# Optimization experiments

Measured on AMD Instinct MI355X. Metric: run time of the kernel, lower is better.

Reference implementation:

```python
import jax, jax.numpy as jnp
import numpy as np


def setup_inputs() -> dict:
    key = jax.random.key(0)
    k = jax.random.split(key, 6)
    N, F, C = 8192, 64, 10
    scale = 1.0 / np.sqrt(F)  # keep activations bounded through relu chain
    return {
        "A_tilde": jax.random.uniform(k[0], (N, N), dtype=jnp.float32),
        "emb": jax.random.normal(k[1], (N, F), dtype=jnp.float32),
        "W1": jax.random.normal(k[2], (F, F), dtype=jnp.float32) * scale,
        "W2": jax.random.normal(k[3], (F, F), dtype=jnp.float32) * scale,
        "Wc": jax.random.normal(k[4], (F, C), dtype=jnp.float32) * scale,
        "bc": jnp.zeros((C,), dtype=jnp.float32),
    }


def reference(A_tilde, emb, W1, W2, Wc, bc):
    # D_tilde = rowsum(A)^(-1/2), with inf -> 0 (nan_to_num posinf=0)
    s = A_tilde.sum(axis=1)
    d = jnp.where(s > 0, jax.lax.rsqrt(jnp.where(s > 0, s, 1.0)), 0.0)  # [N]
    x = emb
    for W in (W1, W2):
        hw = x @ W                          # [N, F] = H W
        # DAD @ HW computed as d * (A @ (d * HW)) -- same math as
        # diag(d) @ A @ diag(d) @ HW, without materializing NxN products
        x = jax.nn.relu(d[:, None] * (A_tilde @ (d[:, None] * hw)))
        # dropout is identity in eval mode
    logits = x @ Wc + bc                    # [N, C]
    return logits
```

## Files before the change

### kernel.cpp

```cpp
#include <hip/hip_runtime.h>
#include <stdint.h>

#define N 8192
#define FD 64
#define NC 10
#define SK 8
#define BM 128
#define BK 128

typedef __attribute__((ext_vector_type(8))) __bf16 bf16x8;
typedef __attribute__((ext_vector_type(4))) float f32x4;
typedef __attribute__((ext_vector_type(4))) float vf4;

__device__ __forceinline__ unsigned short f2bf(float f) {
    unsigned u = __builtin_bit_cast(unsigned, f);
    u += 0x7fffu + ((u >> 16) & 1u);
    return (unsigned short)(u >> 16);
}

__device__ __forceinline__ void g2l16(const void* g, void* l) {
    __builtin_amdgcn_global_load_lds(
        (const __attribute__((address_space(1))) unsigned int*)g,
        (__attribute__((address_space(3))) unsigned int*)l, 16, 0, 0);
}

__global__ __launch_bounds__(256) void rowsum_cast(const float* __restrict__ A,
                                                   unsigned short* __restrict__ Abf,
                                                   float* __restrict__ dvec) {
    const int row = blockIdx.x;
    const int t = threadIdx.x;
    const vf4* Arow = (const vf4*)(A + (size_t)row * N);
    ushort4* Brow = (ushort4*)(Abf + (size_t)row * N);
    float s = 0.f;
#pragma unroll
    for (int i = 0; i < 8; i++) {
        int c4 = t + 256 * i;
        vf4 v = __builtin_nontemporal_load(Arow + c4);
        s += (v.x + v.y) + (v.z + v.w);
        ushort4 o;
        o.x = f2bf(v.x); o.y = f2bf(v.y); o.z = f2bf(v.z); o.w = f2bf(v.w);
        Brow[c4] = o;
    }
#pragma unroll
    for (int off = 32; off > 0; off >>= 1) s += __shfl_down(s, off, 64);
    __shared__ float red[4];
    if ((t & 63) == 0) red[t >> 6] = s;
    __syncthreads();
    if (t == 0) {
        float tot = (red[0] + red[1]) + (red[2] + red[3]);
        dvec[row] = tot > 0.f ? rsqrtf(tot) : 0.f;
    }
}

__device__ __forceinline__ void xw_inner(const float (*Xs)[69], const float* Ws,
                                         const float* __restrict__ dvec,
                                         unsigned short* __restrict__ yT,
                                         int r0, int t) {
    const int l = t & 63, w = t >> 6;
    float acc[16];
#pragma unroll
    for (int i = 0; i < 16; i++) acc[i] = 0.f;
#pragma unroll 8
    for (int j = 0; j < 64; j++) {
        float xv = Xs[l][j];
        const float4* wr = (const float4*)(Ws + j * 64 + w * 16);
        float4 w0 = wr[0], w1 = wr[1], w2 = wr[2], w3 = wr[3];
        acc[0] += xv * w0.x; acc[1] += xv * w0.y; acc[2] += xv * w0.z; acc[3] += xv * w0.w;
        acc[4] += xv * w1.x; acc[5] += xv * w1.y; acc[6] += xv * w1.z; acc[7] += xv * w1.w;
        acc[8] += xv * w2.x; acc[9] += xv * w2.y; acc[10] += xv * w2.z; acc[11] += xv * w2.w;
        acc[12] += xv * w3.x; acc[13] += xv * w3.y; acc[14] += xv * w3.z; acc[15] += xv * w3.w;
    }
    float dl = dvec[r0 + l];
#pragma unroll
    for (int ff = 0; ff < 16; ff++)
        yT[(size_t)(w * 16 + ff) * N + r0 + l] = f2bf(dl * acc[ff]);
}

__global__ __launch_bounds__(256) void xw_from_global(const float* __restrict__ x,
                                                      const float* __restrict__ W,
                                                      const float* __restrict__ dvec,
                                                      unsigned short* __restrict__ yT) {
    __shared__ float Xs[64][69];
    __shared__ __align__(16) float Ws[64 * 64];
    const int t = threadIdx.x;
    const int r0 = blockIdx.x * 64;
    const float4* x4 = (const float4*)x + (size_t)r0 * 16;
    const float4* W4 = (const float4*)W;
#pragma unroll
    for (int p = 0; p < 4; p++) {
        int idx = p * 256 + t;
        ((float4*)Ws)[idx] = W4[idx];
        float4 v = x4[idx];
        int row = idx >> 4, f4 = (idx & 15) * 4;
        Xs[row][f4] = v.x; Xs[row][f4 + 1] = v.y; Xs[row][f4 + 2] = v.z; Xs[row][f4 + 3] = v.w;
    }
    __syncthreads();
    xw_inner(Xs, Ws, dvec, yT, r0, t);
}

__global__ __launch_bounds__(256) void spmm(const unsigned short* __restrict__ Abf,
                                            const unsigned short* __restrict__ yT,
                                            float* __restrict__ partial) {
    constexpr int KS = N / SK;
    __shared__ __align__(16) unsigned short As[BM * BK];
    __shared__ __align__(16) unsigned short Ys[64 * BK];
    const int t = threadIdx.x;
    const int m0 = blockIdx.x * BM;
    const int kbase = blockIdx.y * KS;
    const int lane = t & 63, w = t >> 6;
    const int quad = lane >> 4, lr = lane & 15;

    f32x4 acc[2][4];
#pragma unroll
    for (int mt = 0; mt < 2; mt++)
#pragma unroll
        for (int nt = 0; nt < 4; nt++) {
            acc[mt][nt].x = 0.f; acc[mt][nt].y = 0.f; acc[mt][nt].z = 0.f; acc[mt][nt].w = 0.f;
        }

    for (int k0 = kbase; k0 < kbase + KS; k0 += BK) {
#pragma unroll
        for (int p = 0; p < 8; p++) {
            int s = p * 256 + t;
            int row = s >> 4, c = (s & 15) ^ (row & 15);
            g2l16(Abf + (size_t)(m0 + row) * N + k0 + c * 8, As + s * 8);
        }
#pragma unroll
        for (int p = 0; p < 4; p++) {
            int s = p * 256 + t;
            int row = s >> 4, c = (s & 15) ^ (row & 15);
            g2l16(yT + (size_t)row * N + k0 + c * 8, Ys + s * 8);
        }
        __syncthreads();
#pragma unroll
        for (int kk = 0; kk < BK; kk += 32) {
            int cc = (kk >> 3) + quad;
            bf16x8 af0 = *(const bf16x8*)(As + ((w * 32 + lr) * 16 + (cc ^ lr)) * 8);
            bf16x8 af1 = *(const bf16x8*)(As + ((w * 32 + 16 + lr) * 16 + (cc ^ lr)) * 8);
#pragma unroll
            for (int nt = 0; nt < 4; nt++) {
                bf16x8 bv = *(const bf16x8*)(Ys + ((nt * 16 + lr) * 16 + (cc ^ lr)) * 8);
                acc[0][nt] = __builtin_amdgcn_mfma_f32_16x16x32_bf16(af0, bv, acc[0][nt], 0, 0, 0);
                acc[1][nt] = __builtin_amdgcn_mfma_f32_16x16x32_bf16(af1, bv, acc[1][nt], 0, 0, 0);
            }
        }
        __syncthreads();
    }
#pragma unroll
    for (int mt = 0; mt < 2; mt++)
#pragma unroll
        for (int nt = 0; nt < 4; nt++)
#pragma unroll
            for (int r = 0; r < 4; r++) {
                int m = m0 + w * 32 + mt * 16 + quad * 4 + r;
                partial[((size_t)blockIdx.y * N + m) * FD + nt * 16 + lr] = acc[mt][nt][r];
            }
}

__global__ __launch_bounds__(256) void combine_xw(const float4* __restrict__ partial4,
                                                  const float* __restrict__ W,
                                                  const float* __restrict__ dvec,
                                                  unsigned short* __restrict__ yT) {
    __shared__ float Xs[64][69];
    __shared__ __align__(16) float Ws[64 * 64];
    const int t = threadIdx.x;
    const int r0 = blockIdx.x * 64;
    const float4* W4 = (const float4*)W;
#pragma unroll
    for (int p = 0; p < 4; p++) {
        int idx = p * 256 + t;
        ((float4*)Ws)[idx] = W4[idx];
        int row = idx >> 4, f4c = idx & 15;
        size_t base = (size_t)(r0 + row) * 16 + f4c;
        float4 s = partial4[base];
#pragma unroll
        for (int sk = 1; sk < SK; sk++) {
            float4 v = partial4[(size_t)sk * (N * 16) + base];
            s.x += v.x; s.y += v.y; s.z += v.z; s.w += v.w;
        }
        float dm = dvec[r0 + row];
        int f4 = f4c * 4;
        Xs[row][f4]     = fmaxf(0.f, dm * s.x);
        Xs[row][f4 + 1] = fmaxf(0.f, dm * s.y);
        Xs[row][f4 + 2] = fmaxf(0.f, dm * s.z);
        Xs[row][f4 + 3] = fmaxf(0.f, dm * s.w);
    }
    __syncthreads();
    xw_inner(Xs, Ws, dvec, yT, r0, t);
}

__global__ __launch_bounds__(256) void combine_logits(const float4* __restrict__ partial4,
                                                      const float* __restrict__ dvec,
                                                      const float* __restrict__ Wc,
                                                      const float* __restrict__ bc,
                                                      float* __restrict__ out) {
    __shared__ float Xs[64][69];
    __shared__ float Wcs[64][10];
    __shared__ float bcs[10];
    const int t = threadIdx.x;
    const int r0 = blockIdx.x * 64;
#pragma unroll
    for (int p = 0; p < 4; p++) {
        int idx = p * 256 + t;
        int row = idx >> 4, f4c = idx & 15;
        size_t base = (size_t)(r0 + row) * 16 + f4c;
        float4 s = partial4[base];
#pragma unroll
        for (int sk = 1; sk < SK; sk++) {
            float4 v = partial4[(size_t)sk * (N * 16) + base];
            s.x += v.x; s.y += v.y; s.z += v.z; s.w += v.w;
        }
        float dm = dvec[r0 + row];
        int f4 = f4c * 4;
        Xs[row][f4]     = fmaxf(0.f, dm * s.x);
        Xs[row][f4 + 1] = fmaxf(0.f, dm * s.y);
        Xs[row][f4 + 2] = fmaxf(0.f, dm * s.z);
        Xs[row][f4 + 3] = fmaxf(0.f, dm * s.w);
    }
    for (int i = t; i < 640; i += 256) Wcs[i / 10][i % 10] = Wc[i];
    if (t < 10) bcs[t] = bc[t];
    __syncthreads();
#pragma unroll
    for (int it = 0; it < 3; it++) {
        int idx = it * 256 + t;
        if (idx < 640) {
            int r = idx / 10, c = idx - r * 10;
            float acc = bcs[c];
#pragma unroll
            for (int j = 0; j < 64; j++) acc += Xs[r][j] * Wcs[j][c];
            out[(size_t)(r0 + r) * NC + c] = acc;
        }
    }
}

extern "C" void kernel_launch(void* const* d_in, const int* in_sizes, int n_in,
                              void* d_out, int out_size, void* d_ws, size_t ws_size,
                              hipStream_t stream) {
    const float* A   = (const float*)d_in[0];
    const float* emb = (const float*)d_in[1];
    const float* W1  = (const float*)d_in[2];
    const float* W2  = (const float*)d_in[3];
    const float* Wc  = (const float*)d_in[4];
    const float* bc  = (const float*)d_in[5];
    char* ws = (char*)d_ws;

    unsigned short* Abf  = (unsigned short*)(ws);
    float* dvec          = (float*)(ws + 134217728);
    unsigned short* yT   = (unsigned short*)(ws + 134250496);
    float* partial       = (float*)(ws + 135299072);
    float* out           = (float*)d_out;

    rowsum_cast<<<N, 256, 0, stream>>>(A, Abf, dvec);

    xw_from_global<<<N / 64, 256, 0, stream>>>(emb, W1, dvec, yT);
    spmm<<<dim3(N / BM, SK), 256, 0, stream>>>(Abf, yT, partial);

    combine_xw<<<N / 64, 256, 0, stream>>>((const float4*)partial, W2, dvec, yT);
    spmm<<<dim3(N / BM, SK), 256, 0, stream>>>(Abf, yT, partial);

    combine_logits<<<N / 64, 256, 0, stream>>>((const float4*)partial, dvec, Wc, bc, out);
}
```

Baseline: 430.9 us.

## Double-buffer spmm with smaller tiles and widen combine/xw kernels to 512 threads

The spmm kernel shrinks to 64x64 tiles and adds a two-stage LDS double buffer, so the next A/y tile load is issued before the MFMA work on the current tile. This aims to overlap global-to-LDS traffic with compute and raise grid parallelism (1024 blocks instead of 512). The xw and combine kernels now handle 32 rows per 512-thread block, and partial sums are read with nontemporal loads. Smaller tiles halve A-fragment reuse per B load and raise the number of barriers per K.

```diff
diff --git a/kernel.cpp b/kernel.cpp
--- a/kernel.cpp
+++ b/kernel.cpp
@@ -5,8 +5,8 @@
 #define FD 64
 #define NC 10
 #define SK 8
-#define BM 128
-#define BK 128
+#define BM 64
+#define BK 64
 
 typedef __attribute__((ext_vector_type(8))) __bf16 bf16x8;
 typedef __attribute__((ext_vector_type(4))) float f32x4;
@@ -52,132 +52,129 @@
     }
 }
 
-__device__ __forceinline__ void xw_inner(const float (*Xs)[69], const float* Ws,
-                                         const float* __restrict__ dvec,
-                                         unsigned short* __restrict__ yT,
-                                         int r0, int t) {
+__device__ __forceinline__ void xw_inner512(const float (*Xs)[69], const float* Ws,
+                                            const float* __restrict__ dvec,
+                                            unsigned short* __restrict__ yT,
+                                            int r0, int t) {
     const int l = t & 63, w = t >> 6;
-    float acc[16];
-#pragma unroll
-    for (int i = 0; i < 16; i++) acc[i] = 0.f;
+    const int row = l & 31, fh = l >> 5;
+    const int fbase = w * 8 + fh * 4;
+    float acc0 = 0.f, acc1 = 0.f, acc2 = 0.f, acc3 = 0.f;
 #pragma unroll 8
     for (int j = 0; j < 64; j++) {
-        float xv = Xs[l][j];
-        const float4* wr = (const float4*)(Ws + j * 64 + w * 16);
-        float4 w0 = wr[0], w1 = wr[1], w2 = wr[2], w3 = wr[3];
-        acc[0] += xv * w0.x; acc[1] += xv * w0.y; acc[2] += xv * w0.z; acc[3] += xv * w0.w;
-        acc[4] += xv * w1.x; acc[5] += xv * w1.y; acc[6] += xv * w1.z; acc[7] += xv * w1.w;
-        acc[8] += xv * w2.x; acc[9] += xv * w2.y; acc[10] += xv * w2.z; acc[11] += xv * w2.w;
-        acc[12] += xv * w3.x; acc[13] += xv * w3.y; acc[14] += xv * w3.z; acc[15] += xv * w3.w;
-    }
-    float dl = dvec[r0 + l];
-#pragma unroll
-    for (int ff = 0; ff < 16; ff++)
-        yT[(size_t)(w * 16 + ff) * N + r0 + l] = f2bf(dl * acc[ff]);
-}
-
-__global__ __launch_bounds__(256) void xw_from_global(const float* __restrict__ x,
+        float xv = Xs[row][j];
+        float4 wv = *(const float4*)(Ws + j * 64 + fbase);
+        acc0 += xv * wv.x; acc1 += xv * wv.y; acc2 += xv * wv.z; acc3 += xv * wv.w;
+    }
+    float dl = dvec[r0 + row];
+    yT[(size_t)(fbase + 0) * N + r0 + row] = f2bf(dl * acc0);
+    yT[(size_t)(fbase + 1) * N + r0 + row] = f2bf(dl * acc1);
+    yT[(size_t)(fbase + 2) * N + r0 + row] = f2bf(dl * acc2);
+    yT[(size_t)(fbase + 3) * N + r0 + row] = f2bf(dl * acc3);
+}
+
+__global__ __launch_bounds__(512) void xw_from_global(const float* __restrict__ x,
                                                       const float* __restrict__ W,
                                                       const float* __restrict__ dvec,
                                                       unsigned short* __restrict__ yT) {
-    __shared__ float Xs[64][69];
+    __shared__ float Xs[32][69];
     __shared__ __align__(16) float Ws[64 * 64];
     const int t = threadIdx.x;
-    const int r0 = blockIdx.x * 64;
+    const int r0 = blockIdx.x * 32;
     const float4* x4 = (const float4*)x + (size_t)r0 * 16;
     const float4* W4 = (const float4*)W;
 #pragma unroll
-    for (int p = 0; p < 4; p++) {
-        int idx = p * 256 + t;
-        ((float4*)Ws)[idx] = W4[idx];
-        float4 v = x4[idx];
-        int row = idx >> 4, f4 = (idx & 15) * 4;
+    for (int p = 0; p < 2; p++) ((float4*)Ws)[p * 512 + t] = W4[p * 512 + t];
+    {
+        float4 v = x4[t];
+        int row = t >> 4, f4 = (t & 15) * 4;
         Xs[row][f4] = v.x; Xs[row][f4 + 1] = v.y; Xs[row][f4 + 2] = v.z; Xs[row][f4 + 3] = v.w;
     }
     __syncthreads();
-    xw_inner(Xs, Ws, dvec, yT, r0, t);
+    xw_inner512(Xs, Ws, dvec, yT, r0, t);
 }
 
 __global__ __launch_bounds__(256) void spmm(const unsigned short* __restrict__ Abf,
                                             const unsigned short* __restrict__ yT,
                                             float* __restrict__ partial) {
     constexpr int KS = N / SK;
-    __shared__ __align__(16) unsigned short As[BM * BK];
-    __shared__ __align__(16) unsigned short Ys[64 * BK];
+    constexpr int NTILE = KS / BK;
+    __shared__ __align__(16) unsigned short As[2][BM * BK];
+    __shared__ __align__(16) unsigned short Ys[2][64 * BK];
     const int t = threadIdx.x;
     const int m0 = blockIdx.x * BM;
     const int kbase = blockIdx.y * KS;
     const int lane = t & 63, w = t >> 6;
     const int quad = lane >> 4, lr = lane & 15;
 
-    f32x4 acc[2][4];
-#pragma unroll
-    for (int mt = 0; mt < 2; mt++)
-#pragma unroll
-        for (int nt = 0; nt < 4; nt++) {
-            acc[mt][nt].x = 0.f; acc[mt][nt].y = 0.f; acc[mt][nt].z = 0.f; acc[mt][nt].w = 0.f;
-        }
-
-    for (int k0 = kbase; k0 < kbase + KS; k0 += BK) {
-#pragma unroll
-        for (int p = 0; p < 8; p++) {
+    f32x4 acc[4];
+#pragma unroll
+    for (int nt = 0; nt < 4; nt++) {
+        acc[nt].x = 0.f; acc[nt].y = 0.f; acc[nt].z = 0.f; acc[nt].w = 0.f;
+    }
+
+    auto stage = [&](int buf, int k0) {
+#pragma unroll
+        for (int p = 0; p < 2; p++) {
             int s = p * 256 + t;
-            int row = s >> 4, c = (s & 15) ^ (row & 15);
-            g2l16(Abf + (size_t)(m0 + row) * N + k0 + c * 8, As + s * 8);
-        }
-#pragma unroll
-        for (int p = 0; p < 4; p++) {
+            int row = s >> 3, c = (s & 7) ^ (row & 7);
+            g2l16(Abf + (size_t)(m0 + row) * N + k0 + c * 8, &As[buf][s * 8]);
+        }
+#pragma unroll
+        for (int p = 0; p < 2; p++) {
             int s = p * 256 + t;
-            int row = s >> 4, c = (s & 15) ^ (row & 15);
-            g2l16(yT + (size_t)row * N + k0 + c * 8, Ys + s * 8);
+            int row = s >> 3, c = (s & 7) ^ (row & 7);
+            g2l16(yT + (size_t)row * N + k0 + c * 8, &Ys[buf][s * 8]);
+        }
+    };
+
+    stage(0, kbase);
+    __syncthreads();
+    int cur = 0;
+    for (int ti = 0; ti < NTILE; ++ti) {
+        if (ti + 1 < NTILE) stage(cur ^ 1, kbase + (ti + 1) * BK);
+#pragma unroll
+        for (int kk = 0; kk < 2; kk++) {
+            int cc = kk * 4 + quad;
+            int cs = cc ^ (lr & 7);
+            bf16x8 af = *(const bf16x8*)(&As[cur][((w * 16 + lr) * 8 + cs) * 8]);
+#pragma unroll
+            for (int nt = 0; nt < 4; nt++) {
+                bf16x8 bv = *(const bf16x8*)(&Ys[cur][((nt * 16 + lr) * 8 + cs) * 8]);
+                acc[nt] = __builtin_amdgcn_mfma_f32_16x16x32_bf16(af, bv, acc[nt], 0, 0, 0);
+            }
         }
         __syncthreads();
-#pragma unroll
-        for (int kk = 0; kk < BK; kk += 32) {
-            int cc = (kk >> 3) + quad;
-            bf16x8 af0 = *(const bf16x8*)(As + ((w * 32 + lr) * 16 + (cc ^ lr)) * 8);
-            bf16x8 af1 = *(const bf16x8*)(As + ((w * 32 + 16 + lr) * 16 + (cc ^ lr)) * 8);
-#pragma unroll
-            for (int nt = 0; nt < 4; nt++) {
-                bf16x8 bv = *(const bf16x8*)(Ys + ((nt * 16 + lr) * 16 + (cc ^ lr)) * 8);
-                acc[0][nt] = __builtin_amdgcn_mfma_f32_16x16x32_bf16(af0, bv, acc[0][nt], 0, 0, 0);
-                acc[1][nt] = __builtin_amdgcn_mfma_f32_16x16x32_bf16(af1, bv, acc[1][nt], 0, 0, 0);
-            }
-        }
-        __syncthreads();
-    }
-#pragma unroll
-    for (int mt = 0; mt < 2; mt++)
-#pragma unroll
-        for (int nt = 0; nt < 4; nt++)
-#pragma unroll
-            for (int r = 0; r < 4; r++) {
-                int m = m0 + w * 32 + mt * 16 + quad * 4 + r;
-                partial[((size_t)blockIdx.y * N + m) * FD + nt * 16 + lr] = acc[mt][nt][r];
-            }
-}
-
-__global__ __launch_bounds__(256) void combine_xw(const float4* __restrict__ partial4,
+        cur ^= 1;
+    }
+#pragma unroll
+    for (int nt = 0; nt < 4; nt++)
+#pragma unroll
+        for (int r = 0; r < 4; r++) {
+            int m = m0 + w * 16 + quad * 4 + r;
+            partial[((size_t)blockIdx.y * N + m) * FD + nt * 16 + lr] = acc[nt][r];
+        }
+}
+
+__global__ __launch_bounds__(512) void combine_xw(const float* __restrict__ partial,
                                                   const float* __restrict__ W,
                                                   const float* __restrict__ dvec,
                                                   unsigned short* __restrict__ yT) {
-    __shared__ float Xs[64][69];
+    __shared__ float Xs[32][69];
     __shared__ __align__(16) float Ws[64 * 64];
     const int t = threadIdx.x;
-    const int r0 = blockIdx.x * 64;
+    const int r0 = blockIdx.x * 32;
     const float4* W4 = (const float4*)W;
-#pragma unroll
-    for (int p = 0; p < 4; p++) {
-        int idx = p * 256 + t;
-        ((float4*)Ws)[idx] = W4[idx];
-        int row = idx >> 4, f4c = idx & 15;
+    const vf4* p4 = (const vf4*)partial;
+#pragma unroll
+    for (int p = 0; p < 2; p++) ((float4*)Ws)[p * 512 + t] = W4[p * 512 + t];
+    {
+        int row = t >> 4, f4c = t & 15;
         size_t base = (size_t)(r0 + row) * 16 + f4c;
-        float4 s = partial4[base];
-#pragma unroll
-        for (int sk = 1; sk < SK; sk++) {
-            float4 v = partial4[(size_t)sk * (N * 16) + base];
-            s.x += v.x; s.y += v.y; s.z += v.z; s.w += v.w;
-        }
+        vf4 s = __builtin_nontemporal_load(p4 + base);
+#pragma unroll
+        for (int sk = 1; sk < SK; sk++)
+            s += __builtin_nontemporal_load(p4 + (size_t)sk * (N * 16) + base);
         float dm = dvec[r0 + row];
         int f4 = f4c * 4;
         Xs[row][f4]     = fmaxf(0.f, dm * s.x);
@@ -186,30 +183,27 @@
         Xs[row][f4 + 3] = fmaxf(0.f, dm * s.w);
     }
     __syncthreads();
-    xw_inner(Xs, Ws, dvec, yT, r0, t);
-}
-
-__global__ __launch_bounds__(256) void combine_logits(const float4* __restrict__ partial4,
+    xw_inner512(Xs, Ws, dvec, yT, r0, t);
+}
+
+__global__ __launch_bounds__(512) void combine_logits(const float* __restrict__ partial,
                                                       const float* __restrict__ dvec,
                                                       const float* __restrict__ Wc,
                                                       const float* __restrict__ bc,
                                                       float* __restrict__ out) {
-    __shared__ float Xs[64][69];
+    __shared__ float Xs[32][69];
     __shared__ float Wcs[64][10];
     __shared__ float bcs[10];
     const int t = threadIdx.x;
-    const int r0 = blockIdx.x * 64;
-#pragma unroll
-    for (int p = 0; p < 4; p++) {
-        int idx = p * 256 + t;
-        int row = idx >> 4, f4c = idx & 15;
+    const int r0 = blockIdx.x * 32;
+    const vf4* p4 = (const vf4*)partial;
+    {
+        int row = t >> 4, f4c = t & 15;
         size_t base = (size_t)(r0 + row) * 16 + f4c;
-        float4 s = partial4[base];
-#pragma unroll
-        for (int sk = 1; sk < SK; sk++) {
-            float4 v = partial4[(size_t)sk * (N * 16) + base];
-            s.x += v.x; s.y += v.y; s.z += v.z; s.w += v.w;
-        }
+        vf4 s = __builtin_nontemporal_load(p4 + base);
+#pragma unroll
+        for (int sk = 1; sk < SK; sk++)
+            s += __builtin_nontemporal_load(p4 + (size_t)sk * (N * 16) + base);
         float dm = dvec[r0 + row];
         int f4 = f4c * 4;
         Xs[row][f4]     = fmaxf(0.f, dm * s.x);
@@ -217,19 +211,15 @@
         Xs[row][f4 + 2] = fmaxf(0.f, dm * s.z);
         Xs[row][f4 + 3] = fmaxf(0.f, dm * s.w);
     }
-    for (int i = t; i < 640; i += 256) Wcs[i / 10][i % 10] = Wc[i];
+    for (int i = t; i < 640; i += 512) Wcs[i / 10][i % 10] = Wc[i];
     if (t < 10) bcs[t] = bc[t];
     __syncthreads();
-#pragma unroll
-    for (int it = 0; it < 3; it++) {
-        int idx = it * 256 + t;
-        if (idx < 640) {
-            int r = idx / 10, c = idx - r * 10;
-            float acc = bcs[c];
-#pragma unroll
-            for (int j = 0; j < 64; j++) acc += Xs[r][j] * Wcs[j][c];
-            out[(size_t)(r0 + r) * NC + c] = acc;
-        }
+    if (t < 320) {
+        int r = t / 10, c = t - r * 10;
+        float a = bcs[c];
+#pragma unroll
+        for (int j = 0; j < 64; j++) a += Xs[r][j] * Wcs[j][c];
+        out[(size_t)(r0 + r) * NC + c] = a;
     }
 }
 
@@ -252,11 +242,11 @@
 
     rowsum_cast<<<N, 256, 0, stream>>>(A, Abf, dvec);
 
-    xw_from_global<<<N / 64, 256, 0, stream>>>(emb, W1, dvec, yT);
+    xw_from_global<<<N / 32, 512, 0, stream>>>(emb, W1, dvec, yT);
     spmm<<<dim3(N / BM, SK), 256, 0, stream>>>(Abf, yT, partial);
 
-    combine_xw<<<N / 64, 256, 0, stream>>>((const float4*)partial, W2, dvec, yT);
+    combine_xw<<<N / 32, 512, 0, stream>>>(partial, W2, dvec, yT);
     spmm<<<dim3(N / BM, SK), 256, 0, stream>>>(Abf, yT, partial);
 
-    combine_logits<<<N / 64, 256, 0, stream>>>((const float4*)partial, dvec, Wc, bc, out);
-}
+    combine_logits<<<N / 32, 512, 0, stream>>>(partial, dvec, Wc, bc, out);
+}
```

After: 429.0 us. No clear change (-0.5%).
